# Kernel tuning notes

Measured on AMD Instinct MI355X. Metric: run time of the kernel, lower is better.

## Reference

```python
import jax, jax.numpy as jnp
import numpy as np

HID = 512
HEADS = 8
HEAD_DIM = HID // HEADS


def setup_inputs() -> dict:
    key = jax.random.key(0)
    ks = jax.random.split(key, 12)
    B, S = 2, 2048
    inp = {
        "q": jax.random.normal(ks[0], (B, S, HID), jnp.float32),
        "k": jax.random.normal(ks[1], (B, S, HID), jnp.float32),
        "v": jax.random.normal(ks[2], (B, S, HID), jnp.float32),
        "mask": jnp.ones((B, 1, S, S), jnp.int32),
    }
    s = 1.0 / np.sqrt(HID)
    inp["Wq"] = jax.random.uniform(ks[3], (HID, HID), jnp.float32, -s, s)
    inp["bq"] = jax.random.uniform(ks[4], (HID,), jnp.float32, -s, s)
    inp["Wk"] = jax.random.uniform(ks[5], (HID, HID), jnp.float32, -s, s)
    inp["bk"] = jax.random.uniform(ks[6], (HID,), jnp.float32, -s, s)
    inp["Wv"] = jax.random.uniform(ks[7], (HID, HID), jnp.float32, -s, s)
    inp["bv"] = jax.random.uniform(ks[8], (HID,), jnp.float32, -s, s)
    inp["Wo"] = jax.random.uniform(ks[9], (HID, HID), jnp.float32, -s, s)
    inp["bo"] = jax.random.uniform(ks[10], (HID,), jnp.float32, -s, s)
    return inp


def _split_heads(x, B):
    # [B, S, HID] -> [B, H, S, D]
    return x.reshape(B, -1, HEADS, HEAD_DIM).transpose(0, 2, 1, 3)


def reference(q, k, v, mask, Wq, bq, Wk, bk, Wv, bv, Wo, bo):
    B = q.shape[0]
    qh = _split_heads(q @ Wq.T + bq, B)
    kh = _split_heads(k @ Wk.T + bk, B)
    vh = _split_heads(v @ Wv.T + bv, B)
    scale = 1.0 / jnp.sqrt(jnp.float32(HEAD_DIM))
    # [B, H, S, S] score matrix (explicitly materialized, as in source)
    scores = jnp.einsum("bhqd,bhkd->bhqk", qh, kh) * scale
    scores = jnp.where(mask == 0, jnp.float32(-1e10), scores)
    attn = jax.nn.softmax(scores, axis=-1)
    x = jnp.einsum("bhqk,bhkd->bhqd", attn, vh)  # dropout p=0 -> identity
    x = x.transpose(0, 2, 1, 3).reshape(B, -1, HID)
    out = x @ Wo.T + bo
    return out, attn
```

## Files before the change

### kernel.cpp

```cpp
#include <hip/hip_runtime.h>
#include <math.h>

#define BB   2
#define SS   2048
#define HH   8
#define DD   64
#define HIDD 512
#define NT   (BB * SS)

typedef _Float16 half8   __attribute__((ext_vector_type(8)));
typedef _Float16 half4_t __attribute__((ext_vector_type(4)));
typedef float    f32x4   __attribute__((ext_vector_type(4)));

__device__ __forceinline__ f32x4 mfma16(half8 a, half8 b, f32x4 c) {
    return __builtin_amdgcn_mfma_f32_16x16x32_f16(a, b, c, 0, 0, 0);
}

__device__ __forceinline__ void split_store(float4 v, _Float16* hp, _Float16* lp) {
    half4_t hv, lv;
    hv[0] = (_Float16)v.x; lv[0] = (_Float16)(v.x - (float)hv[0]);
    hv[1] = (_Float16)v.y; lv[1] = (_Float16)(v.y - (float)hv[1]);
    hv[2] = (_Float16)v.z; lv[2] = (_Float16)(v.z - (float)hv[2]);
    hv[3] = (_Float16)v.w; lv[3] = (_Float16)(v.w - (float)hv[3]);
    *(half4_t*)hp = hv;
    *(half4_t*)lp = lv;
}

#define PADK 40
template <int MODE>
__global__ __launch_bounds__(256) void proj_mfma(const float* __restrict__ X,
                                                 const float* __restrict__ W,
                                                 const float* __restrict__ bias,
                                                 float* __restrict__ Y) {
    alignas(16) __shared__ _Float16 Xh[64][PADK], Xl[64][PADK];
    alignas(16) __shared__ _Float16 Wh[64][PADK], Wl[64][PADK];

    const int tid = threadIdx.x;
    const int w  = tid >> 6;
    const int l  = tid & 63;
    const int lm = l & 15;
    const int lg = l >> 4;
    const int row0 = blockIdx.x * 64;
    const int col0 = blockIdx.y * 64;

    f32x4 acc[4];
#pragma unroll
    for (int nt = 0; nt < 4; ++nt) acc[nt] = f32x4{0.f, 0.f, 0.f, 0.f};

    for (int kk = 0; kk < HIDD; kk += 32) {
        __syncthreads();
#pragma unroll
        for (int p = 0; p < 2; ++p) {
            const int idx = tid + p * 256;
            const int r = idx >> 3, c4 = idx & 7;
            float4 xv = *(const float4*)&X[(size_t)(row0 + r) * HIDD + kk + c4 * 4];
            split_store(xv, &Xh[r][c4 * 4], &Xl[r][c4 * 4]);
            float4 wv = *(const float4*)&W[(size_t)(col0 + r) * HIDD + kk + c4 * 4];
            split_store(wv, &Wh[r][c4 * 4], &Wl[r][c4 * 4]);
        }
        __syncthreads();

        half8 ah = *(const half8*)&Xh[w * 16 + lm][lg * 8];
        half8 al = *(const half8*)&Xl[w * 16 + lm][lg * 8];
#pragma unroll
        for (int nt = 0; nt < 4; ++nt) {
            half8 bh = *(const half8*)&Wh[nt * 16 + lm][lg * 8];
            half8 bl = *(const half8*)&Wl[nt * 16 + lm][lg * 8];
            acc[nt] = mfma16(ah, bh, acc[nt]);
            acc[nt] = mfma16(ah, bl, acc[nt]);
            acc[nt] = mfma16(al, bh, acc[nt]);
        }
    }

    if constexpr (MODE == 2) {
        __shared__ float Ts[64][65];
        __syncthreads();
#pragma unroll
        for (int nt = 0; nt < 4; ++nt) {
            const float bv = bias[col0 + nt * 16 + lm];
#pragma unroll
            for (int r = 0; r < 4; ++r)
                Ts[w * 16 + lg * 4 + r][nt * 16 + lm] = acc[nt][r] + bv;
        }
        __syncthreads();
        const int c  = tid >> 2;
        const int sb = (tid & 3) * 16;
        const int b  = row0 >> 11;
        const int h  = col0 >> 6;
        float* dst = Y + (((size_t)b * HH + h) * DD + c) * SS + (row0 & (SS - 1));
#pragma unroll
        for (int u = 0; u < 4; ++u) {
            const int s0 = sb + u * 4;
            float4 o = {Ts[s0][c], Ts[s0 + 1][c], Ts[s0 + 2][c], Ts[s0 + 3][c]};
            *(float4*)&dst[s0] = o;
        }
    } else {
#pragma unroll
        for (int nt = 0; nt < 4; ++nt) {
            const int ncol = col0 + nt * 16 + lm;
            const float bv = bias[ncol];
#pragma unroll
            for (int r = 0; r < 4; ++r) {
                const int mrow = row0 + w * 16 + lg * 4 + r;
                const float val = acc[nt][r] + bv;
                if (MODE == 0) {
                    const int b = mrow >> 11, s = mrow & (SS - 1);
                    const int h = ncol >> 6, d = ncol & 63;
                    Y[(((size_t)b * HH + h) * SS + s) * DD + d] = val;
                } else {
                    Y[(size_t)mrow * HIDD + ncol] = val;
                }
            }
        }
    }
}

#define PADD 72
__global__ __launch_bounds__(256) void scores_mfma(
    const float* __restrict__ qh, const float* __restrict__ kh,
    const int* __restrict__ mask, float* __restrict__ attn,
    float* __restrict__ mstat, float* __restrict__ lstat) {
    alignas(16) __shared__ _Float16 Qh[64][PADD], Ql[64][PADD];
    alignas(16) __shared__ _Float16 Kh[64][PADD], Kl[64][PADD];

    const int tid = threadIdx.x;
    const int w  = tid >> 6;
    const int l  = tid & 63;
    const int lm = l & 15;
    const int lg = l >> 4;
    const int bh = blockIdx.y;
    const int b  = bh >> 3;
    const int q0 = blockIdx.x * 64;

    {
        const float* qsrc = qh + ((size_t)bh * SS + q0) * DD;
#pragma unroll
        for (int p = 0; p < 4; ++p) {
            const int idx = tid + p * 256;
            const int r = idx >> 4, c4 = idx & 15;
            float4 v = *(const float4*)&qsrc[(size_t)r * DD + c4 * 4];
            split_store(v, &Qh[r][c4 * 4], &Ql[r][c4 * 4]);
        }
    }

    float mreg[4], lsum[4];
#pragma unroll
    for (int r = 0; r < 4; ++r) { mreg[r] = -INFINITY; lsum[r] = 0.f; }

    for (int k0 = 0; k0 < SS; k0 += 64) {
        __syncthreads();
        {
            const float* ksrc = kh + ((size_t)bh * SS + k0) * DD;
#pragma unroll
            for (int p = 0; p < 4; ++p) {
                const int idx = tid + p * 256;
                const int r = idx >> 4, c4 = idx & 15;
                float4 v = *(const float4*)&ksrc[(size_t)r * DD + c4 * 4];
                split_store(v, &Kh[r][c4 * 4], &Kl[r][c4 * 4]);
            }
        }
        __syncthreads();

        half8 ah[2], al[2];
#pragma unroll
        for (int ks = 0; ks < 2; ++ks) {
            ah[ks] = *(const half8*)&Qh[w * 16 + lm][ks * 32 + lg * 8];
            al[ks] = *(const half8*)&Ql[w * 16 + lm][ks * 32 + lg * 8];
        }

        float sv[4][4];
#pragma unroll
        for (int nt = 0; nt < 4; ++nt) {
            f32x4 sacc = f32x4{0.f, 0.f, 0.f, 0.f};
#pragma unroll
            for (int ks = 0; ks < 2; ++ks) {
                half8 bhv = *(const half8*)&Kh[nt * 16 + lm][ks * 32 + lg * 8];
                half8 blv = *(const half8*)&Kl[nt * 16 + lm][ks * 32 + lg * 8];
                sacc = mfma16(ah[ks], bhv, sacc);
                sacc = mfma16(ah[ks], blv, sacc);
                sacc = mfma16(al[ks], bhv, sacc);
            }
#pragma unroll
            for (int r = 0; r < 4; ++r) {
                const int q  = q0 + w * 16 + lg * 4 + r;
                const int kp = k0 + nt * 16 + lm;
                const int mk = mask[((size_t)b * SS + q) * SS + kp];
                const float s = mk ? sacc[r] * 0.125f : -1e10f;
                attn[((size_t)bh * SS + q) * SS + kp] = s;
                sv[nt][r] = s;
            }
        }
#pragma unroll
        for (int r = 0; r < 4; ++r) {
            float tm = fmaxf(fmaxf(sv[0][r], sv[1][r]), fmaxf(sv[2][r], sv[3][r]));
#pragma unroll
            for (int d = 1; d < 16; d <<= 1) tm = fmaxf(tm, __shfl_xor(tm, d, 64));
            const float mn = fmaxf(mreg[r], tm);
            float ps = __expf(sv[0][r] - mn) + __expf(sv[1][r] - mn) +
                       __expf(sv[2][r] - mn) + __expf(sv[3][r] - mn);
#pragma unroll
            for (int d = 1; d < 16; d <<= 1) ps += __shfl_xor(ps, d, 64);
            lsum[r] = lsum[r] * __expf(mreg[r] - mn) + ps;
            mreg[r] = mn;
        }
    }

    if (lm == 0) {
#pragma unroll
        for (int r = 0; r < 4; ++r) {
            const int q = q0 + w * 16 + lg * 4 + r;
            mstat[(size_t)bh * SS + q] = mreg[r];
            lstat[(size_t)bh * SS + q] = lsum[r];
        }
    }
}

__global__ __launch_bounds__(256) void pv_mfma(
    const float* __restrict__ vt, float* __restrict__ attn,
    const float* __restrict__ mstat, const float* __restrict__ lstat,
    float* __restrict__ xbuf) {
    alignas(16) __shared__ _Float16 Vh[64][PADD], Vl[64][PADD];

    const int tid = threadIdx.x;
    const int w  = tid >> 6;
    const int l  = tid & 63;
    const int lm = l & 15;
    const int lg = l >> 4;
    const int bh = blockIdx.y;
    const int b  = bh >> 3;
    const int h  = bh & 7;
    const int q0 = blockIdx.x * 64;

    const int q_a = q0 + w * 16 + lm;
    const float mreg = mstat[(size_t)bh * SS + q_a];
    const float rl   = 1.0f / lstat[(size_t)bh * SS + q_a];
    const size_t arow = ((size_t)bh * SS + q_a) * SS;

    f32x4 acc[4];
#pragma unroll
    for (int nt = 0; nt < 4; ++nt) acc[nt] = f32x4{0.f, 0.f, 0.f, 0.f};

    for (int k0 = 0; k0 < SS; k0 += 64) {
        __syncthreads();
        {
            const float* vsrc = vt + (size_t)bh * DD * SS + k0;
#pragma unroll
            for (int p = 0; p < 4; ++p) {
                const int idx = tid + p * 256;
                const int r = idx >> 4, c4 = idx & 15;
                float4 v = *(const float4*)&vsrc[(size_t)r * SS + c4 * 4];
                split_store(v, &Vh[r][c4 * 4], &Vl[r][c4 * 4]);
            }
        }
        __syncthreads();

        half8 phi[2], plo[2];
#pragma unroll
        for (int ks = 0; ks < 2; ++ks) {
            const size_t base = arow + k0 + ks * 32 + lg * 8;
            float4 s0 = *(const float4*)&attn[base];
            float4 s1 = *(const float4*)&attn[base + 4];
            float4 p0, p1;
            p0.x = __expf(s0.x - mreg) * rl;
            p0.y = __expf(s0.y - mreg) * rl;
            p0.z = __expf(s0.z - mreg) * rl;
            p0.w = __expf(s0.w - mreg) * rl;
            p1.x = __expf(s1.x - mreg) * rl;
            p1.y = __expf(s1.y - mreg) * rl;
            p1.z = __expf(s1.z - mreg) * rl;
            p1.w = __expf(s1.w - mreg) * rl;
            *(float4*)&attn[base]     = p0;
            *(float4*)&attn[base + 4] = p1;
            half8 ph, pl;
            ph[0] = (_Float16)p0.x; pl[0] = (_Float16)(p0.x - (float)ph[0]);
            ph[1] = (_Float16)p0.y; pl[1] = (_Float16)(p0.y - (float)ph[1]);
            ph[2] = (_Float16)p0.z; pl[2] = (_Float16)(p0.z - (float)ph[2]);
            ph[3] = (_Float16)p0.w; pl[3] = (_Float16)(p0.w - (float)ph[3]);
            ph[4] = (_Float16)p1.x; pl[4] = (_Float16)(p1.x - (float)ph[4]);
            ph[5] = (_Float16)p1.y; pl[5] = (_Float16)(p1.y - (float)ph[5]);
            ph[6] = (_Float16)p1.z; pl[6] = (_Float16)(p1.z - (float)ph[6]);
            ph[7] = (_Float16)p1.w; pl[7] = (_Float16)(p1.w - (float)ph[7]);
            phi[ks] = ph; plo[ks] = pl;
        }

#pragma unroll
        for (int nt = 0; nt < 4; ++nt) {
#pragma unroll
            for (int ks = 0; ks < 2; ++ks) {
                half8 vh8 = *(const half8*)&Vh[nt * 16 + lm][ks * 32 + lg * 8];
                half8 vl8 = *(const half8*)&Vl[nt * 16 + lm][ks * 32 + lg * 8];
                acc[nt] = mfma16(phi[ks], vh8, acc[nt]);
                acc[nt] = mfma16(phi[ks], vl8, acc[nt]);
                acc[nt] = mfma16(plo[ks], vh8, acc[nt]);
            }
        }
    }

#pragma unroll
    for (int nt = 0; nt < 4; ++nt) {
#pragma unroll
        for (int r = 0; r < 4; ++r) {
            const int q = q0 + w * 16 + lg * 4 + r;
            xbuf[((size_t)b * SS + q) * HIDD + h * DD + nt * 16 + lm] = acc[nt][r];
        }
    }
}

extern "C" void kernel_launch(void* const* d_in, const int* in_sizes, int n_in,
                              void* d_out, int out_size, void* d_ws,
                              size_t ws_size, hipStream_t stream) {
    const float* q  = (const float*)d_in[0];
    const float* k  = (const float*)d_in[1];
    const float* v  = (const float*)d_in[2];
    const int* mask = (const int*)d_in[3];
    const float* Wq = (const float*)d_in[4];
    const float* bq = (const float*)d_in[5];
    const float* Wk = (const float*)d_in[6];
    const float* bk = (const float*)d_in[7];
    const float* Wv = (const float*)d_in[8];
    const float* bv = (const float*)d_in[9];
    const float* Wo = (const float*)d_in[10];
    const float* bo = (const float*)d_in[11];

    float* out  = (float*)d_out;
    float* attn = out + (size_t)BB * SS * HIDD;

    float* ws    = (float*)d_ws;
    float* qh    = ws;
    float* kh    = qh + (size_t)BB * HH * SS * DD;
    float* vt    = kh + (size_t)BB * HH * SS * DD;
    float* xbuf  = vt + (size_t)BB * HH * DD * SS;
    float* mstat = xbuf + (size_t)BB * SS * HIDD;
    float* lstat = mstat + (size_t)BB * HH * SS;

    dim3 gproj(NT / 64, HIDD / 64);
    proj_mfma<0><<<gproj, 256, 0, stream>>>(q, Wq, bq, qh);
    proj_mfma<0><<<gproj, 256, 0, stream>>>(k, Wk, bk, kh);
    proj_mfma<2><<<gproj, 256, 0, stream>>>(v, Wv, bv, vt);

    dim3 gattn(SS / 64, BB * HH);
    scores_mfma<<<gattn, 256, 0, stream>>>(qh, kh, mask, attn, mstat, lstat);
    pv_mfma<<<gattn, 256, 0, stream>>>(vt, attn, mstat, lstat, xbuf);

    proj_mfma<1><<<gproj, 256, 0, stream>>>(xbuf, Wo, bo, out);
}
```

Before: 668.6 us.

## Pre-split inputs to fp16 hi/lo in global memory and drop LDS staging

Adds separate split kernels that convert inputs and weights into fp16 high/low pairs once, so each GEMM kernel loads fp16 fragments straight from global memory with no shared-memory staging or block barriers. The attention kernels now give each lane a query row, which vectorizes mask and score stores as float4. Q is pre-scaled in the projection. Intermediates are stored as fp16 hi/lo pairs, which removes repeated splitting of K and V tiles inside every block. The cost is seven extra launches and extra global traffic, and uncoalesced per-lane fragment loads could increase cache pressure.

```diff
diff --git a/kernel.cpp b/kernel.cpp
--- a/kernel.cpp
+++ b/kernel.cpp
@@ -16,293 +16,230 @@
     return __builtin_amdgcn_mfma_f32_16x16x32_f16(a, b, c, 0, 0, 0);
 }
 
-__device__ __forceinline__ void split_store(float4 v, _Float16* hp, _Float16* lp) {
-    half4_t hv, lv;
-    hv[0] = (_Float16)v.x; lv[0] = (_Float16)(v.x - (float)hv[0]);
-    hv[1] = (_Float16)v.y; lv[1] = (_Float16)(v.y - (float)hv[1]);
-    hv[2] = (_Float16)v.z; lv[2] = (_Float16)(v.z - (float)hv[2]);
-    hv[3] = (_Float16)v.w; lv[3] = (_Float16)(v.w - (float)hv[3]);
-    *(half4_t*)hp = hv;
-    *(half4_t*)lp = lv;
-}
-
-#define PADK 40
-template <int MODE>
-__global__ __launch_bounds__(256) void proj_mfma(const float* __restrict__ X,
-                                                 const float* __restrict__ W,
-                                                 const float* __restrict__ bias,
-                                                 float* __restrict__ Y) {
-    alignas(16) __shared__ _Float16 Xh[64][PADK], Xl[64][PADK];
-    alignas(16) __shared__ _Float16 Wh[64][PADK], Wl[64][PADK];
-
+__global__ __launch_bounds__(256) void split_kernel(const float* __restrict__ src,
+                                                    _Float16* __restrict__ dh,
+                                                    _Float16* __restrict__ dl,
+                                                    int n4) {
+    for (int i = blockIdx.x * 256 + threadIdx.x; i < n4; i += gridDim.x * 256) {
+        float4 v = ((const float4*)src)[i];
+        half4_t h, l;
+        h[0] = (_Float16)v.x; l[0] = (_Float16)(v.x - (float)h[0]);
+        h[1] = (_Float16)v.y; l[1] = (_Float16)(v.y - (float)h[1]);
+        h[2] = (_Float16)v.z; l[2] = (_Float16)(v.z - (float)h[2]);
+        h[3] = (_Float16)v.w; l[3] = (_Float16)(v.w - (float)h[3]);
+        ((half4_t*)dh)[i] = h;
+        ((half4_t*)dl)[i] = l;
+    }
+}
+
+template <int OMODE>
+__global__ __launch_bounds__(256) void proj_f16(
+    const _Float16* __restrict__ Xh, const _Float16* __restrict__ Xl,
+    const _Float16* __restrict__ Wh, const _Float16* __restrict__ Wl,
+    const float* __restrict__ bias, _Float16* __restrict__ Yh,
+    _Float16* __restrict__ Yl, float* __restrict__ Yf, float scale) {
     const int tid = threadIdx.x;
-    const int w  = tid >> 6;
-    const int l  = tid & 63;
-    const int lm = l & 15;
-    const int lg = l >> 4;
-    const int row0 = blockIdx.x * 64;
+    const int w = tid >> 6, l = tid & 63, lm = l & 15, lg = l >> 4;
+    const int row  = blockIdx.x * 64 + w * 16 + lm;
     const int col0 = blockIdx.y * 64;
 
+    const _Float16* xh = Xh + (size_t)row * HIDD;
+    const _Float16* xl = Xl + (size_t)row * HIDD;
+
     f32x4 acc[4];
 #pragma unroll
-    for (int nt = 0; nt < 4; ++nt) acc[nt] = f32x4{0.f, 0.f, 0.f, 0.f};
+    for (int mt = 0; mt < 4; ++mt) acc[mt] = f32x4{0.f, 0.f, 0.f, 0.f};
 
     for (int kk = 0; kk < HIDD; kk += 32) {
-        __syncthreads();
-#pragma unroll
-        for (int p = 0; p < 2; ++p) {
-            const int idx = tid + p * 256;
-            const int r = idx >> 3, c4 = idx & 7;
-            float4 xv = *(const float4*)&X[(size_t)(row0 + r) * HIDD + kk + c4 * 4];
-            split_store(xv, &Xh[r][c4 * 4], &Xl[r][c4 * 4]);
-            float4 wv = *(const float4*)&W[(size_t)(col0 + r) * HIDD + kk + c4 * 4];
-            split_store(wv, &Wh[r][c4 * 4], &Wl[r][c4 * 4]);
-        }
-        __syncthreads();
-
-        half8 ah = *(const half8*)&Xh[w * 16 + lm][lg * 8];
-        half8 al = *(const half8*)&Xl[w * 16 + lm][lg * 8];
-#pragma unroll
-        for (int nt = 0; nt < 4; ++nt) {
-            half8 bh = *(const half8*)&Wh[nt * 16 + lm][lg * 8];
-            half8 bl = *(const half8*)&Wl[nt * 16 + lm][lg * 8];
-            acc[nt] = mfma16(ah, bh, acc[nt]);
-            acc[nt] = mfma16(ah, bl, acc[nt]);
-            acc[nt] = mfma16(al, bh, acc[nt]);
-        }
-    }
-
-    if constexpr (MODE == 2) {
-        __shared__ float Ts[64][65];
-        __syncthreads();
-#pragma unroll
-        for (int nt = 0; nt < 4; ++nt) {
-            const float bv = bias[col0 + nt * 16 + lm];
-#pragma unroll
-            for (int r = 0; r < 4; ++r)
-                Ts[w * 16 + lg * 4 + r][nt * 16 + lm] = acc[nt][r] + bv;
-        }
-        __syncthreads();
-        const int c  = tid >> 2;
-        const int sb = (tid & 3) * 16;
-        const int b  = row0 >> 11;
-        const int h  = col0 >> 6;
-        float* dst = Y + (((size_t)b * HH + h) * DD + c) * SS + (row0 & (SS - 1));
-#pragma unroll
-        for (int u = 0; u < 4; ++u) {
-            const int s0 = sb + u * 4;
-            float4 o = {Ts[s0][c], Ts[s0 + 1][c], Ts[s0 + 2][c], Ts[s0 + 3][c]};
-            *(float4*)&dst[s0] = o;
-        }
-    } else {
-#pragma unroll
-        for (int nt = 0; nt < 4; ++nt) {
-            const int ncol = col0 + nt * 16 + lm;
-            const float bv = bias[ncol];
+        half8 bhv = *(const half8*)&xh[kk + lg * 8];
+        half8 blv = *(const half8*)&xl[kk + lg * 8];
+#pragma unroll
+        for (int mt = 0; mt < 4; ++mt) {
+            const size_t woff = (size_t)(col0 + mt * 16 + lm) * HIDD + kk + lg * 8;
+            half8 ah = *(const half8*)&Wh[woff];
+            half8 al = *(const half8*)&Wl[woff];
+            acc[mt] = mfma16(ah, bhv, acc[mt]);
+            acc[mt] = mfma16(ah, blv, acc[mt]);
+            acc[mt] = mfma16(al, bhv, acc[mt]);
+        }
+    }
+
+    const int b = row >> 11, s = row & (SS - 1);
+    const int hcol = col0 >> 6;
+#pragma unroll
+    for (int mt = 0; mt < 4; ++mt) {
+        const int d0 = mt * 16 + lg * 4;
+        float4 bv = *(const float4*)&bias[col0 + d0];
+        float vals[4];
+#pragma unroll
+        for (int r = 0; r < 4; ++r) vals[r] = (acc[mt][r] + ((const float*)&bv)[r]) * scale;
+
+        if constexpr (OMODE == 2) {
+            float4 o = {vals[0], vals[1], vals[2], vals[3]};
+            *(float4*)&Yf[(size_t)row * HIDD + col0 + d0] = o;
+        } else {
+            half4_t hv, lv;
 #pragma unroll
             for (int r = 0; r < 4; ++r) {
-                const int mrow = row0 + w * 16 + lg * 4 + r;
-                const float val = acc[nt][r] + bv;
-                if (MODE == 0) {
-                    const int b = mrow >> 11, s = mrow & (SS - 1);
-                    const int h = ncol >> 6, d = ncol & 63;
-                    Y[(((size_t)b * HH + h) * SS + s) * DD + d] = val;
-                } else {
-                    Y[(size_t)mrow * HIDD + ncol] = val;
+                hv[r] = (_Float16)vals[r];
+                lv[r] = (_Float16)(vals[r] - (float)hv[r]);
+            }
+            if constexpr (OMODE == 0) {
+                const size_t dst = (((size_t)b * HH + hcol) * SS + s) * DD + d0;
+                *(half4_t*)&Yh[dst] = hv;
+                *(half4_t*)&Yl[dst] = lv;
+            } else {
+#pragma unroll
+                for (int r = 0; r < 4; ++r) {
+                    const size_t dst = (((size_t)b * HH + hcol) * DD + d0 + r) * SS + s;
+                    Yh[dst] = hv[r];
+                    Yl[dst] = lv[r];
                 }
             }
         }
     }
 }
 
-#define PADD 72
-__global__ __launch_bounds__(256) void scores_mfma(
-    const float* __restrict__ qh, const float* __restrict__ kh,
+__global__ __launch_bounds__(256) void scores_f16(
+    const _Float16* __restrict__ qph, const _Float16* __restrict__ qpl,
+    const _Float16* __restrict__ kph, const _Float16* __restrict__ kpl,
     const int* __restrict__ mask, float* __restrict__ attn,
     float* __restrict__ mstat, float* __restrict__ lstat) {
-    alignas(16) __shared__ _Float16 Qh[64][PADD], Ql[64][PADD];
-    alignas(16) __shared__ _Float16 Kh[64][PADD], Kl[64][PADD];
-
     const int tid = threadIdx.x;
-    const int w  = tid >> 6;
-    const int l  = tid & 63;
-    const int lm = l & 15;
-    const int lg = l >> 4;
-    const int bh = blockIdx.y;
-    const int b  = bh >> 3;
-    const int q0 = blockIdx.x * 64;
-
-    {
-        const float* qsrc = qh + ((size_t)bh * SS + q0) * DD;
-#pragma unroll
-        for (int p = 0; p < 4; ++p) {
-            const int idx = tid + p * 256;
-            const int r = idx >> 4, c4 = idx & 15;
-            float4 v = *(const float4*)&qsrc[(size_t)r * DD + c4 * 4];
-            split_store(v, &Qh[r][c4 * 4], &Ql[r][c4 * 4]);
-        }
-    }
-
-    float mreg[4], lsum[4];
-#pragma unroll
-    for (int r = 0; r < 4; ++r) { mreg[r] = -INFINITY; lsum[r] = 0.f; }
+    const int w = tid >> 6, l = tid & 63, lm = l & 15, lg = l >> 4;
+    const int bh = blockIdx.y, b = bh >> 3;
+    const int q = blockIdx.x * 64 + w * 16 + lm;
+
+    const size_t qoff = ((size_t)bh * SS + q) * DD;
+    half8 qfh[2], qfl[2];
+#pragma unroll
+    for (int ks = 0; ks < 2; ++ks) {
+        qfh[ks] = *(const half8*)&qph[qoff + ks * 32 + lg * 8];
+        qfl[ks] = *(const half8*)&qpl[qoff + ks * 32 + lg * 8];
+    }
+
+    const int* mrow = mask + ((size_t)b * SS + q) * SS;
+    float* arow = attn + ((size_t)bh * SS + q) * SS;
+    const _Float16* kb_h = kph + (size_t)bh * SS * DD;
+    const _Float16* kb_l = kpl + (size_t)bh * SS * DD;
+
+    float m = -INFINITY, lsum = 0.f;
 
     for (int k0 = 0; k0 < SS; k0 += 64) {
-        __syncthreads();
-        {
-            const float* ksrc = kh + ((size_t)bh * SS + k0) * DD;
-#pragma unroll
-            for (int p = 0; p < 4; ++p) {
-                const int idx = tid + p * 256;
-                const int r = idx >> 4, c4 = idx & 15;
-                float4 v = *(const float4*)&ksrc[(size_t)r * DD + c4 * 4];
-                split_store(v, &Kh[r][c4 * 4], &Kl[r][c4 * 4]);
-            }
-        }
-        __syncthreads();
-
-        half8 ah[2], al[2];
+        float sv[16];
+#pragma unroll
+        for (int kt = 0; kt < 4; ++kt) {
+            const size_t koff = (size_t)(k0 + kt * 16 + lm) * DD;
+            f32x4 sacc = f32x4{0.f, 0.f, 0.f, 0.f};
+#pragma unroll
+            for (int ks = 0; ks < 2; ++ks) {
+                half8 ah = *(const half8*)&kb_h[koff + ks * 32 + lg * 8];
+                half8 al = *(const half8*)&kb_l[koff + ks * 32 + lg * 8];
+                sacc = mfma16(ah, qfh[ks], sacc);
+                sacc = mfma16(ah, qfl[ks], sacc);
+                sacc = mfma16(al, qfh[ks], sacc);
+            }
+            int4 mk = *(const int4*)&mrow[k0 + kt * 16 + lg * 4];
+            float4 s4;
+            s4.x = mk.x ? sacc[0] : -1e10f;
+            s4.y = mk.y ? sacc[1] : -1e10f;
+            s4.z = mk.z ? sacc[2] : -1e10f;
+            s4.w = mk.w ? sacc[3] : -1e10f;
+            *(float4*)&arow[k0 + kt * 16 + lg * 4] = s4;
+            sv[kt * 4 + 0] = s4.x; sv[kt * 4 + 1] = s4.y;
+            sv[kt * 4 + 2] = s4.z; sv[kt * 4 + 3] = s4.w;
+        }
+        float tmax = sv[0];
+#pragma unroll
+        for (int i = 1; i < 16; ++i) tmax = fmaxf(tmax, sv[i]);
+        tmax = fmaxf(tmax, __shfl_xor(tmax, 16, 64));
+        tmax = fmaxf(tmax, __shfl_xor(tmax, 32, 64));
+        const float mn = fmaxf(m, tmax);
+        float ps = 0.f;
+#pragma unroll
+        for (int i = 0; i < 16; ++i) ps += __expf(sv[i] - mn);
+        ps += __shfl_xor(ps, 16, 64);
+        ps += __shfl_xor(ps, 32, 64);
+        lsum = lsum * __expf(m - mn) + ps;
+        m = mn;
+    }
+
+    if (lg == 0) {
+        mstat[(size_t)bh * SS + q] = m;
+        lstat[(size_t)bh * SS + q] = lsum;
+    }
+}
+
+__global__ __launch_bounds__(256) void pv_f16(
+    const _Float16* __restrict__ vth, const _Float16* __restrict__ vtl,
+    float* __restrict__ attn, const float* __restrict__ mstat,
+    const float* __restrict__ lstat, _Float16* __restrict__ xh,
+    _Float16* __restrict__ xl) {
+    const int tid = threadIdx.x;
+    const int w = tid >> 6, l = tid & 63, lm = l & 15, lg = l >> 4;
+    const int bh = blockIdx.y, b = bh >> 3, h = bh & 7;
+    const int q = blockIdx.x * 64 + w * 16 + lm;
+
+    const float m  = mstat[(size_t)bh * SS + q];
+    const float rl = 1.0f / lstat[(size_t)bh * SS + q];
+    float* arow = attn + ((size_t)bh * SS + q) * SS;
+    const _Float16* vb_h = vth + (size_t)bh * DD * SS;
+    const _Float16* vb_l = vtl + (size_t)bh * DD * SS;
+
+    f32x4 acc[4];
+#pragma unroll
+    for (int nt = 0; nt < 4; ++nt) acc[nt] = f32x4{0.f, 0.f, 0.f, 0.f};
+
+    for (int k0 = 0; k0 < SS; k0 += 64) {
+        half8 pfh[2], pfl[2];
 #pragma unroll
         for (int ks = 0; ks < 2; ++ks) {
-            ah[ks] = *(const half8*)&Qh[w * 16 + lm][ks * 32 + lg * 8];
-            al[ks] = *(const half8*)&Ql[w * 16 + lm][ks * 32 + lg * 8];
-        }
-
-        float sv[4][4];
+            const int cb = k0 + ks * 32 + lg * 8;
+            float4 s0 = *(const float4*)&arow[cb];
+            float4 s1 = *(const float4*)&arow[cb + 4];
+            float p[8];
+            p[0] = __expf(s0.x - m) * rl; p[1] = __expf(s0.y - m) * rl;
+            p[2] = __expf(s0.z - m) * rl; p[3] = __expf(s0.w - m) * rl;
+            p[4] = __expf(s1.x - m) * rl; p[5] = __expf(s1.y - m) * rl;
+            p[6] = __expf(s1.z - m) * rl; p[7] = __expf(s1.w - m) * rl;
+            float4 o0 = {p[0], p[1], p[2], p[3]};
+            float4 o1 = {p[4], p[5], p[6], p[7]};
+            *(float4*)&arow[cb]     = o0;
+            *(float4*)&arow[cb + 4] = o1;
+            half8 ph, pl;
+#pragma unroll
+            for (int i = 0; i < 8; ++i) {
+                ph[i] = (_Float16)p[i];
+                pl[i] = (_Float16)(p[i] - (float)ph[i]);
+            }
+            pfh[ks] = ph; pfl[ks] = pl;
+        }
 #pragma unroll
         for (int nt = 0; nt < 4; ++nt) {
-            f32x4 sacc = f32x4{0.f, 0.f, 0.f, 0.f};
 #pragma unroll
             for (int ks = 0; ks < 2; ++ks) {
-                half8 bhv = *(const half8*)&Kh[nt * 16 + lm][ks * 32 + lg * 8];
-                half8 blv = *(const half8*)&Kl[nt * 16 + lm][ks * 32 + lg * 8];
-                sacc = mfma16(ah[ks], bhv, sacc);
-                sacc = mfma16(ah[ks], blv, sacc);
-                sacc = mfma16(al[ks], bhv, sacc);
-            }
-#pragma unroll
-            for (int r = 0; r < 4; ++r) {
-                const int q  = q0 + w * 16 + lg * 4 + r;
-                const int kp = k0 + nt * 16 + lm;
-                const int mk = mask[((size_t)b * SS + q) * SS + kp];
-                const float s = mk ? sacc[r] * 0.125f : -1e10f;
-                attn[((size_t)bh * SS + q) * SS + kp] = s;
-                sv[nt][r] = s;
-            }
-        }
+                const size_t voff = (size_t)(nt * 16 + lm) * SS + k0 + ks * 32 + lg * 8;
+                half8 vh = *(const half8*)&vb_h[voff];
+                half8 vl = *(const half8*)&vb_l[voff];
+                acc[nt] = mfma16(vh, pfh[ks], acc[nt]);
+                acc[nt] = mfma16(vh, pfl[ks], acc[nt]);
+                acc[nt] = mfma16(vl, pfh[ks], acc[nt]);
+            }
+        }
+    }
+
+#pragma unroll
+    for (int nt = 0; nt < 4; ++nt) {
+        half4_t hv, lv;
 #pragma unroll
         for (int r = 0; r < 4; ++r) {
-            float tm = fmaxf(fmaxf(sv[0][r], sv[1][r]), fmaxf(sv[2][r], sv[3][r]));
-#pragma unroll
-            for (int d = 1; d < 16; d <<= 1) tm = fmaxf(tm, __shfl_xor(tm, d, 64));
-            const float mn = fmaxf(mreg[r], tm);
-            float ps = __expf(sv[0][r] - mn) + __expf(sv[1][r] - mn) +
-                       __expf(sv[2][r] - mn) + __expf(sv[3][r] - mn);
-#pragma unroll
-            for (int d = 1; d < 16; d <<= 1) ps += __shfl_xor(ps, d, 64);
-            lsum[r] = lsum[r] * __expf(mreg[r] - mn) + ps;
-            mreg[r] = mn;
-        }
-    }
-
-    if (lm == 0) {
-#pragma unroll
-        for (int r = 0; r < 4; ++r) {
-            const int q = q0 + w * 16 + lg * 4 + r;
-            mstat[(size_t)bh * SS + q] = mreg[r];
-            lstat[(size_t)bh * SS + q] = lsum[r];
-        }
-    }
-}
-
-__global__ __launch_bounds__(256) void pv_mfma(
-    const float* __restrict__ vt, float* __restrict__ attn,
-    const float* __restrict__ mstat, const float* __restrict__ lstat,
-    float* __restrict__ xbuf) {
-    alignas(16) __shared__ _Float16 Vh[64][PADD], Vl[64][PADD];
-
-    const int tid = threadIdx.x;
-    const int w  = tid >> 6;
-    const int l  = tid & 63;
-    const int lm = l & 15;
-    const int lg = l >> 4;
-    const int bh = blockIdx.y;
-    const int b  = bh >> 3;
-    const int h  = bh & 7;
-    const int q0 = blockIdx.x * 64;
-
-    const int q_a = q0 + w * 16 + lm;
-    const float mreg = mstat[(size_t)bh * SS + q_a];
-    const float rl   = 1.0f / lstat[(size_t)bh * SS + q_a];
-    const size_t arow = ((size_t)bh * SS + q_a) * SS;
-
-    f32x4 acc[4];
-#pragma unroll
-    for (int nt = 0; nt < 4; ++nt) acc[nt] = f32x4{0.f, 0.f, 0.f, 0.f};
-
-    for (int k0 = 0; k0 < SS; k0 += 64) {
-        __syncthreads();
-        {
-            const float* vsrc = vt + (size_t)bh * DD * SS + k0;
-#pragma unroll
-            for (int p = 0; p < 4; ++p) {
-                const int idx = tid + p * 256;
-                const int r = idx >> 4, c4 = idx & 15;
-                float4 v = *(const float4*)&vsrc[(size_t)r * SS + c4 * 4];
-                split_store(v, &Vh[r][c4 * 4], &Vl[r][c4 * 4]);
-            }
-        }
-        __syncthreads();
-
-        half8 phi[2], plo[2];
-#pragma unroll
-        for (int ks = 0; ks < 2; ++ks) {
-            const size_t base = arow + k0 + ks * 32 + lg * 8;
-            float4 s0 = *(const float4*)&attn[base];
-            float4 s1 = *(const float4*)&attn[base + 4];
-            float4 p0, p1;
-            p0.x = __expf(s0.x - mreg) * rl;
-            p0.y = __expf(s0.y - mreg) * rl;
-            p0.z = __expf(s0.z - mreg) * rl;
-            p0.w = __expf(s0.w - mreg) * rl;
-            p1.x = __expf(s1.x - mreg) * rl;
-            p1.y = __expf(s1.y - mreg) * rl;
-            p1.z = __expf(s1.z - mreg) * rl;
-            p1.w = __expf(s1.w - mreg) * rl;
-            *(float4*)&attn[base]     = p0;
-            *(float4*)&attn[base + 4] = p1;
-            half8 ph, pl;
-            ph[0] = (_Float16)p0.x; pl[0] = (_Float16)(p0.x - (float)ph[0]);
-            ph[1] = (_Float16)p0.y; pl[1] = (_Float16)(p0.y - (float)ph[1]);
-            ph[2] = (_Float16)p0.z; pl[2] = (_Float16)(p0.z - (float)ph[2]);
-            ph[3] = (_Float16)p0.w; pl[3] = (_Float16)(p0.w - (float)ph[3]);
-            ph[4] = (_Float16)p1.x; pl[4] = (_Float16)(p1.x - (float)ph[4]);
-            ph[5] = (_Float16)p1.y; pl[5] = (_Float16)(p1.y - (float)ph[5]);
-            ph[6] = (_Float16)p1.z; pl[6] = (_Float16)(p1.z - (float)ph[6]);
-            ph[7] = (_Float16)p1.w; pl[7] = (_Float16)(p1.w - (float)ph[7]);
-            phi[ks] = ph; plo[ks] = pl;
-        }
-
-#pragma unroll
-        for (int nt = 0; nt < 4; ++nt) {
-#pragma unroll
-            for (int ks = 0; ks < 2; ++ks) {
-                half8 vh8 = *(const half8*)&Vh[nt * 16 + lm][ks * 32 + lg * 8];
-                half8 vl8 = *(const half8*)&Vl[nt * 16 + lm][ks * 32 + lg * 8];
-                acc[nt] = mfma16(phi[ks], vh8, acc[nt]);
-                acc[nt] = mfma16(phi[ks], vl8, acc[nt]);
-                acc[nt] = mfma16(plo[ks], vh8, acc[nt]);
-            }
-        }
-    }
-
-#pragma unroll
-    for (int nt = 0; nt < 4; ++nt) {
-#pragma unroll
-        for (int r = 0; r < 4; ++r) {
-            const int q = q0 + w * 16 + lg * 4 + r;
-            xbuf[((size_t)b * SS + q) * HIDD + h * DD + nt * 16 + lm] = acc[nt][r];
-        }
+            const float val = acc[nt][r];
+            hv[r] = (_Float16)val;
+            lv[r] = (_Float16)(val - (float)hv[r]);
+        }
+        const size_t dst = ((size_t)b * SS + q) * HIDD + h * DD + nt * 16 + lg * 4;
+        *(half4_t*)&xh[dst] = hv;
+        *(half4_t*)&xl[dst] = lv;
     }
 }
 
@@ -325,22 +262,45 @@
     float* out  = (float*)d_out;
     float* attn = out + (size_t)BB * SS * HIDD;
 
-    float* ws    = (float*)d_ws;
-    float* qh    = ws;
-    float* kh    = qh + (size_t)BB * HH * SS * DD;
-    float* vt    = kh + (size_t)BB * HH * SS * DD;
-    float* xbuf  = vt + (size_t)BB * HH * DD * SS;
-    float* mstat = xbuf + (size_t)BB * SS * HIDD;
+    const size_t NE = (size_t)NT * HIDD;
+    const size_t WE = (size_t)HIDD * HIDD;
+
+    _Float16* p = (_Float16*)d_ws;
+    _Float16 *qsh = p, *qsl = qsh + NE, *ksh = qsl + NE, *ksl = ksh + NE;
+    _Float16 *vsh = ksl + NE, *vsl = vsh + NE;
+    p = vsl + NE;
+    _Float16 *wqh = p, *wql = wqh + WE, *wkh = wql + WE, *wkl = wkh + WE;
+    _Float16 *wvh = wkl + WE, *wvl = wvh + WE, *woh = wvl + WE, *wol = woh + WE;
+    p = wol + WE;
+    _Float16 *qph = p, *qpl = qph + NE, *kph = qpl + NE, *kpl = kph + NE;
+    _Float16 *vth = kpl + NE, *vtl = vth + NE;
+    _Float16 *xh = vtl + NE, *xl = xh + NE;
+    p = xl + NE;
+    float* mstat = (float*)p;
     float* lstat = mstat + (size_t)BB * HH * SS;
 
+    const int n4i = (int)(NE / 4), n4w = (int)(WE / 4);
+    split_kernel<<<2048, 256, 0, stream>>>(q, qsh, qsl, n4i);
+    split_kernel<<<2048, 256, 0, stream>>>(k, ksh, ksl, n4i);
+    split_kernel<<<2048, 256, 0, stream>>>(v, vsh, vsl, n4i);
+    split_kernel<<<256, 256, 0, stream>>>(Wq, wqh, wql, n4w);
+    split_kernel<<<256, 256, 0, stream>>>(Wk, wkh, wkl, n4w);
+    split_kernel<<<256, 256, 0, stream>>>(Wv, wvh, wvl, n4w);
+    split_kernel<<<256, 256, 0, stream>>>(Wo, woh, wol, n4w);
+
     dim3 gproj(NT / 64, HIDD / 64);
-    proj_mfma<0><<<gproj, 256, 0, stream>>>(q, Wq, bq, qh);
-    proj_mfma<0><<<gproj, 256, 0, stream>>>(k, Wk, bk, kh);
-    proj_mfma<2><<<gproj, 256, 0, stream>>>(v, Wv, bv, vt);
+    proj_f16<0><<<gproj, 256, 0, stream>>>(qsh, qsl, wqh, wql, bq, qph, qpl,
+                                           nullptr, 0.125f);
+    proj_f16<0><<<gproj, 256, 0, stream>>>(ksh, ksl, wkh, wkl, bk, kph, kpl,
+                                           nullptr, 1.0f);
+    proj_f16<1><<<gproj, 256, 0, stream>>>(vsh, vsl, wvh, wvl, bv, vth, vtl,
+                                           nullptr, 1.0f);
 
     dim3 gattn(SS / 64, BB * HH);
-    scores_mfma<<<gattn, 256, 0, stream>>>(qh, kh, mask, attn, mstat, lstat);
-    pv_mfma<<<gattn, 256, 0, stream>>>(vt, attn, mstat, lstat, xbuf);
-
-    proj_mfma<1><<<gproj, 256, 0, stream>>>(xbuf, Wo, bo, out);
-}
+    scores_f16<<<gattn, 256, 0, stream>>>(qph, qpl, kph, kpl, mask, attn,
+                                          mstat, lstat);
+    pv_f16<<<gattn, 256, 0, stream>>>(vth, vtl, attn, mstat, lstat, xh, xl);
+
+    proj_f16<2><<<gproj, 256, 0, stream>>>(xh, xl, woh, wol, bo, nullptr,
+                                           nullptr, out, 1.0f);
+}
```

Measured after the change: 866.5 us. 29.6% more time.
